# Performance work log

Measured on AMD Instinct MI355X. Metric: run time of the kernel, lower is better.

The kernel has to match this reference:

```python
import jax, jax.numpy as jnp
import numpy as np

B, N = 262144, 64
CLIP_RATIO = 0.2
DUAL_CLIP = 5.0
USE_VALUE_CLIP = True
HALF_LOG_2PI = 0.5 * float(np.log(2.0 * np.pi))


def setup_inputs() -> dict:
    key = jax.random.key(0)
    ks = jax.random.split(key, 9)
    return {
        "mu_new": jax.random.normal(ks[0], (B, N), jnp.float32),
        "sigma_new": jax.random.uniform(ks[1], (B, N), jnp.float32, 0.5, 1.5),
        "mu_old": jax.random.normal(ks[2], (B, N), jnp.float32),
        "sigma_old": jax.random.uniform(ks[3], (B, N), jnp.float32, 0.5, 1.5),
        "action": jax.random.normal(ks[4], (B, N), jnp.float32),
        "value_new": jax.random.normal(ks[5], (B,), jnp.float32),
        "value_old": jax.random.normal(ks[6], (B,), jnp.float32),
        "adv": jax.random.normal(ks[7], (B,), jnp.float32),
        "return_": jax.random.normal(ks[8], (B,), jnp.float32),
        "weight": jnp.ones((B,), jnp.float32),
    }


def _gauss_logprob(action, mu, sigma):
    # independent Normal log-prob, summed over action dim -> (B,)
    z = (action - mu) / sigma
    return jnp.sum(-0.5 * z * z - jnp.log(sigma) - HALF_LOG_2PI, axis=-1)


def reference(mu_new, sigma_new, mu_old, sigma_old, action,
              value_new, value_old, adv, return_, weight):
    logp_new = _gauss_logprob(action, mu_new, sigma_new)   # (B,)
    logp_old = _gauss_logprob(action, mu_old, sigma_old)   # (B,) constant w.r.t. new params
    ratio = jnp.exp(logp_new - logp_old)

    surr1 = ratio * adv
    surr2 = jnp.clip(ratio, 1.0 - CLIP_RATIO, 1.0 + CLIP_RATIO) * adv
    clipped = jnp.minimum(surr1, surr2)
    # dual clip (arXiv:1912.09729 Eq. 5)
    clipped = jnp.maximum(clipped, DUAL_CLIP * adv)
    policy_loss = -jnp.mean(clipped * weight)

    # entropy of diagonal Gaussian, summed over N
    entropy = jnp.sum(0.5 + HALF_LOG_2PI + jnp.log(sigma_new), axis=-1)
    entropy_loss = jnp.mean(entropy * weight)

    if USE_VALUE_CLIP:
        value_clip = value_old + jnp.clip(value_new - value_old, -CLIP_RATIO, CLIP_RATIO)
        v1 = jnp.square(return_ - value_new)
        v2 = jnp.square(return_ - value_clip)
        value_loss = 0.5 * jnp.mean(jnp.maximum(v1, v2) * weight)
    else:
        value_loss = 0.5 * jnp.mean(jnp.square(return_ - value_new) * weight)

    approx_kl = jnp.mean(logp_old - logp_new)
    clipfrac = jnp.mean((jnp.abs(ratio - 1.0) > CLIP_RATIO).astype(jnp.float32))
    return policy_loss, value_loss, entropy_loss, approx_kl, clipfrac
```

## Files before the change

### kernel.cpp

```cpp
#include <hip/hip_runtime.h>

static constexpr int   N_DIM        = 64;
static constexpr float HALF_LOG_2PI = 0.9189385332046727f;
static constexpr float CLIP_RATIO   = 0.2f;
static constexpr float DUAL_CLIP    = 5.0f;
static constexpr int   GRID         = 2048;

__global__ __launch_bounds__(256) void ppo_main(
    const float* __restrict__ mu_new,
    const float* __restrict__ sg_new,
    const float* __restrict__ mu_old,
    const float* __restrict__ sg_old,
    const float* __restrict__ act,
    const float* __restrict__ vnew,
    const float* __restrict__ vold,
    const float* __restrict__ adv,
    const float* __restrict__ ret,
    const float* __restrict__ wgt,
    float* __restrict__ ws,
    int n_groups, int b_rows)
{
    const int t    = threadIdx.x;
    const int wave = t >> 6;
    const int lane = t & 63;
    const int sub  = lane >> 4;
    const int sl   = lane & 15;

    float accP = 0.f, accV = 0.f, accE = 0.f, accK = 0.f, accC = 0.f;

    {
        const int gtid = blockIdx.x * 256 + t;
        const int tot  = gridDim.x * 256;
        for (int r = gtid; r < b_rows; r += tot) {
            const float vn = vnew[r], vo = vold[r], rt = ret[r], w = wgt[r];
            const float vc = vo + fminf(fmaxf(vn - vo, -CLIP_RATIO), CLIP_RATIO);
            const float d1 = rt - vn, d2 = rt - vc;
            accV += fmaxf(d1 * d1, d2 * d2) * w;
        }
    }

    for (int g = blockIdx.x; g < n_groups; g += gridDim.x) {
        const int base_row = g * 16 + wave * 4;
        const int off      = base_row * N_DIM + lane * 4;

        const float4 mn = *(const float4*)(mu_new + off);
        const float4 sn = *(const float4*)(sg_new + off);
        const float4 mo = *(const float4*)(mu_old + off);
        const float4 so = *(const float4*)(sg_old + off);
        const float4 a  = *(const float4*)(act    + off);

        float w = 0.f, ad = 0.f;
        if (sl == 0) {
            const int r = base_row + sub;
            w  = wgt[r];
            ad = adv[r];
        }

        float qn = 0.f, qo = 0.f, en = 0.f, eo = 0.f;
#define PPO_COMP(c) {                                        \
        float rn = __builtin_amdgcn_rcpf(sn.c);              \
        float zn = (a.c - mn.c) * rn;  qn += zn * zn;        \
        float ro = __builtin_amdgcn_rcpf(so.c);              \
        float zo = (a.c - mo.c) * ro;  qo += zo * zo;        \
        en += __logf(sn.c);  eo += __logf(so.c); }
        PPO_COMP(x) PPO_COMP(y) PPO_COMP(z) PPO_COMP(w)
#undef PPO_COMP

        float pn = -0.5f * qn - en;
        float po = -0.5f * qo - eo;

#pragma unroll
        for (int m = 1; m < 16; m <<= 1) {
            pn += __shfl_xor(pn, m, 16);
            po += __shfl_xor(po, m, 16);
            en += __shfl_xor(en, m, 16);
        }

        if (sl == 0) {
            const float ratio = __expf(pn - po);
            const float s1 = ratio * ad;
            const float rc = fminf(fmaxf(ratio, 1.0f - CLIP_RATIO), 1.0f + CLIP_RATIO);
            const float s2 = rc * ad;
            float cl = fminf(s1, s2);
            cl = fmaxf(cl, DUAL_CLIP * ad);
            accP += cl * w;

            accE += ((float)N_DIM * (0.5f + HALF_LOG_2PI) + en) * w;
            accK += (po - pn);
            accC += (fabsf(ratio - 1.0f) > CLIP_RATIO) ? 1.0f : 0.0f;
        }
    }

#pragma unroll
    for (int m = 1; m < 64; m <<= 1) accV += __shfl_xor(accV, m, 64);
#pragma unroll
    for (int m = 16; m < 64; m <<= 1) {
        accP += __shfl_xor(accP, m, 64);
        accE += __shfl_xor(accE, m, 64);
        accK += __shfl_xor(accK, m, 64);
        accC += __shfl_xor(accC, m, 64);
    }

    __shared__ float red[4][5];
    if (lane == 0) {
        red[wave][0] = accP; red[wave][1] = accV; red[wave][2] = accE;
        red[wave][3] = accK; red[wave][4] = accC;
    }
    __syncthreads();

    if (t == 0) {
        float s[5] = {0.f, 0.f, 0.f, 0.f, 0.f};
#pragma unroll
        for (int wv = 0; wv < 4; ++wv)
#pragma unroll
            for (int k = 0; k < 5; ++k) s[k] += red[wv][k];
#pragma unroll
        for (int k = 0; k < 5; ++k) ws[k * GRID + blockIdx.x] = s[k];
    }
}

__global__ __launch_bounds__(256) void ppo_reduce(
    const float* __restrict__ ws, float* __restrict__ out, int b_rows)
{
    const int t    = threadIdx.x;
    const int wave = t >> 6;
    const int lane = t & 63;
    __shared__ float red[4];

    const float invB = 1.0f / (float)b_rows;

    for (int k = 0; k < 5; ++k) {
        float v = 0.f;
        for (int i = t; i < GRID; i += 256) v += ws[k * GRID + i];
#pragma unroll
        for (int m = 1; m < 64; m <<= 1) v += __shfl_xor(v, m, 64);
        if (lane == 0) red[wave] = v;
        __syncthreads();
        if (t == 0) {
            float s = red[0] + red[1] + red[2] + red[3];
            float o;
            if      (k == 0) o = -s * invB;
            else if (k == 1) o = 0.5f * s * invB;
            else             o = s * invB;
            out[k] = o;
        }
        __syncthreads();
    }
}

extern "C" void kernel_launch(void* const* d_in, const int* in_sizes, int n_in,
                              void* d_out, int out_size, void* d_ws, size_t ws_size,
                              hipStream_t stream) {
    const float* mu_new = (const float*)d_in[0];
    const float* sg_new = (const float*)d_in[1];
    const float* mu_old = (const float*)d_in[2];
    const float* sg_old = (const float*)d_in[3];
    const float* act    = (const float*)d_in[4];
    const float* vnew   = (const float*)d_in[5];
    const float* vold   = (const float*)d_in[6];
    const float* adv    = (const float*)d_in[7];
    const float* ret    = (const float*)d_in[8];
    const float* wgt    = (const float*)d_in[9];
    float* out = (float*)d_out;
    float* ws  = (float*)d_ws;

    const int b_rows   = in_sizes[5];
    const int n_groups = b_rows / 16;

    ppo_main<<<GRID, 256, 0, stream>>>(mu_new, sg_new, mu_old, sg_old, act,
                                       vnew, vold, adv, ret, wgt,
                                       ws, n_groups, b_rows);
    ppo_reduce<<<1, 256, 0, stream>>>(ws, out, b_rows);
}
```

Measured before the change: 322.9 us.

## Process two row sets per iteration and cut shuffle reductions in PPO loss

Each wave now handles 8 rows per loop iteration instead of 4, issuing ten float4 loads at once to put more memory requests in flight. Only the log-ratio difference goes through the 16-lane shuffle reduction. Entropy and KL are accumulated per lane, and the ratio terms are computed redundantly on all lanes, then scaled by 1/16. The value-loss loop becomes a single guarded pass, which assumes the grid covers every row. The final reduce kernel uses one wave per output instead of looping with barriers.

```diff
diff --git a/kernel.cpp b/kernel.cpp
--- a/kernel.cpp
+++ b/kernel.cpp
@@ -5,6 +5,26 @@
 static constexpr float CLIP_RATIO   = 0.2f;
 static constexpr float DUAL_CLIP    = 5.0f;
 static constexpr int   GRID         = 2048;
+static constexpr float ENT_CONST    = (float)N_DIM * (0.5f + HALF_LOG_2PI);
+static constexpr float ENT_C16      = ENT_CONST / 16.0f;
+
+__device__ __forceinline__ void ppo_set(const float4& mn, const float4& sn,
+                                        const float4& mo, const float4& so,
+                                        const float4& a,
+                                        float& en_out, float& d_out)
+{
+    float qn = 0.f, qo = 0.f, en = 0.f, eo = 0.f;
+#define PPO_COMP(c) {                                        \
+        float rn = __builtin_amdgcn_rcpf(sn.c);              \
+        float zn = (a.c - mn.c) * rn;  qn += zn * zn;        \
+        float ro = __builtin_amdgcn_rcpf(so.c);              \
+        float zo = (a.c - mo.c) * ro;  qo += zo * zo;        \
+        en += __logf(sn.c);  eo += __logf(so.c); }
+    PPO_COMP(x) PPO_COMP(y) PPO_COMP(z) PPO_COMP(w)
+#undef PPO_COMP
+    en_out = en;
+    d_out  = 0.5f * (qo - qn) + (eo - en);
+}
 
 __global__ __launch_bounds__(256) void ppo_main(
     const float* __restrict__ mu_new,
@@ -18,20 +38,18 @@
     const float* __restrict__ ret,
     const float* __restrict__ wgt,
     float* __restrict__ ws,
-    int n_groups, int b_rows)
+    int b_rows)
 {
     const int t    = threadIdx.x;
     const int wave = t >> 6;
     const int lane = t & 63;
     const int sub  = lane >> 4;
-    const int sl   = lane & 15;
 
     float accP = 0.f, accV = 0.f, accE = 0.f, accK = 0.f, accC = 0.f;
 
     {
-        const int gtid = blockIdx.x * 256 + t;
-        const int tot  = gridDim.x * 256;
-        for (int r = gtid; r < b_rows; r += tot) {
+        const int r = blockIdx.x * 256 + t;
+        if (r < b_rows) {
             const float vn = vnew[r], vo = vold[r], rt = ret[r], w = wgt[r];
             const float vc = vo + fminf(fmaxf(vn - vo, -CLIP_RATIO), CLIP_RATIO);
             const float d1 = rt - vn, d2 = rt - vc;
@@ -39,63 +57,65 @@
         }
     }
 
-    for (int g = blockIdx.x; g < n_groups; g += gridDim.x) {
-        const int base_row = g * 16 + wave * 4;
-        const int off      = base_row * N_DIM + lane * 4;
+    const int n_g = b_rows >> 5;
+    for (int g = blockIdx.x; g < n_g; g += gridDim.x) {
+        const int row0 = g * 32 + wave * 8;
+        const int r0   = row0 + sub;
+        const int r1   = r0 + 4;
+        const int off0 = row0 * N_DIM + lane * 4;
+        const int off1 = off0 + 4 * N_DIM;
 
-        const float4 mn = *(const float4*)(mu_new + off);
-        const float4 sn = *(const float4*)(sg_new + off);
-        const float4 mo = *(const float4*)(mu_old + off);
-        const float4 so = *(const float4*)(sg_old + off);
-        const float4 a  = *(const float4*)(act    + off);
+        const float4 mn0 = *(const float4*)(mu_new + off0);
+        const float4 sn0 = *(const float4*)(sg_new + off0);
+        const float4 mo0 = *(const float4*)(mu_old + off0);
+        const float4 so0 = *(const float4*)(sg_old + off0);
+        const float4 a0  = *(const float4*)(act    + off0);
+        const float4 mn1 = *(const float4*)(mu_new + off1);
+        const float4 sn1 = *(const float4*)(sg_new + off1);
+        const float4 mo1 = *(const float4*)(mu_old + off1);
+        const float4 so1 = *(const float4*)(sg_old + off1);
+        const float4 a1  = *(const float4*)(act    + off1);
+        const float w0 = wgt[r0], ad0 = adv[r0];
+        const float w1 = wgt[r1], ad1 = adv[r1];
 
-        float w = 0.f, ad = 0.f;
-        if (sl == 0) {
-            const int r = base_row + sub;
-            w  = wgt[r];
-            ad = adv[r];
-        }
+        float en0, d0, en1, d1;
+        ppo_set(mn0, sn0, mo0, so0, a0, en0, d0);
+        ppo_set(mn1, sn1, mo1, so1, a1, en1, d1);
 
-        float qn = 0.f, qo = 0.f, en = 0.f, eo = 0.f;
-#define PPO_COMP(c) {                                        \
-        float rn = __builtin_amdgcn_rcpf(sn.c);              \
-        float zn = (a.c - mn.c) * rn;  qn += zn * zn;        \
-        float ro = __builtin_amdgcn_rcpf(so.c);              \
-        float zo = (a.c - mo.c) * ro;  qo += zo * zo;        \
-        en += __logf(sn.c);  eo += __logf(so.c); }
-        PPO_COMP(x) PPO_COMP(y) PPO_COMP(z) PPO_COMP(w)
-#undef PPO_COMP
-
-        float pn = -0.5f * qn - en;
-        float po = -0.5f * qo - eo;
+        accK -= (d0 + d1);
+        accE += w0 * (en0 + ENT_C16) + w1 * (en1 + ENT_C16);
 
 #pragma unroll
         for (int m = 1; m < 16; m <<= 1) {
-            pn += __shfl_xor(pn, m, 16);
-            po += __shfl_xor(po, m, 16);
-            en += __shfl_xor(en, m, 16);
+            d0 += __shfl_xor(d0, m, 16);
+            d1 += __shfl_xor(d1, m, 16);
         }
 
-        if (sl == 0) {
-            const float ratio = __expf(pn - po);
-            const float s1 = ratio * ad;
-            const float rc = fminf(fmaxf(ratio, 1.0f - CLIP_RATIO), 1.0f + CLIP_RATIO);
-            const float s2 = rc * ad;
-            float cl = fminf(s1, s2);
-            cl = fmaxf(cl, DUAL_CLIP * ad);
-            accP += cl * w;
-
-            accE += ((float)N_DIM * (0.5f + HALF_LOG_2PI) + en) * w;
-            accK += (po - pn);
-            accC += (fabsf(ratio - 1.0f) > CLIP_RATIO) ? 1.0f : 0.0f;
+        {
+            const float ratio = __expf(d0);
+            const float rc = fminf(fmaxf(ratio, 1.f - CLIP_RATIO), 1.f + CLIP_RATIO);
+            float cl = fminf(ratio * ad0, rc * ad0);
+            cl = fmaxf(cl, DUAL_CLIP * ad0);
+            accP += cl * w0;
+            accC += (fabsf(ratio - 1.f) > CLIP_RATIO) ? 1.f : 0.f;
+        }
+        {
+            const float ratio = __expf(d1);
+            const float rc = fminf(fmaxf(ratio, 1.f - CLIP_RATIO), 1.f + CLIP_RATIO);
+            float cl = fminf(ratio * ad1, rc * ad1);
+            cl = fmaxf(cl, DUAL_CLIP * ad1);
+            accP += cl * w1;
+            accC += (fabsf(ratio - 1.f) > CLIP_RATIO) ? 1.f : 0.f;
         }
     }
 
+    accP *= 0.0625f;
+    accC *= 0.0625f;
+
 #pragma unroll
-    for (int m = 1; m < 64; m <<= 1) accV += __shfl_xor(accV, m, 64);
-#pragma unroll
-    for (int m = 16; m < 64; m <<= 1) {
+    for (int m = 1; m < 64; m <<= 1) {
         accP += __shfl_xor(accP, m, 64);
+        accV += __shfl_xor(accV, m, 64);
         accE += __shfl_xor(accE, m, 64);
         accK += __shfl_xor(accK, m, 64);
         accC += __shfl_xor(accC, m, 64);
@@ -119,32 +139,24 @@
     }
 }
 
-__global__ __launch_bounds__(256) void ppo_reduce(
+__global__ __launch_bounds__(320) void ppo_reduce(
     const float* __restrict__ ws, float* __restrict__ out, int b_rows)
 {
-    const int t    = threadIdx.x;
-    const int wave = t >> 6;
-    const int lane = t & 63;
-    __shared__ float red[4];
+    const int wave = threadIdx.x >> 6;
+    const int lane = threadIdx.x & 63;
 
-    const float invB = 1.0f / (float)b_rows;
+    float v = 0.f;
+    for (int i = lane; i < GRID; i += 64) v += ws[wave * GRID + i];
+#pragma unroll
+    for (int m = 1; m < 64; m <<= 1) v += __shfl_xor(v, m, 64);
 
-    for (int k = 0; k < 5; ++k) {
-        float v = 0.f;
-        for (int i = t; i < GRID; i += 256) v += ws[k * GRID + i];
-#pragma unroll
-        for (int m = 1; m < 64; m <<= 1) v += __shfl_xor(v, m, 64);
-        if (lane == 0) red[wave] = v;
-        __syncthreads();
-        if (t == 0) {
-            float s = red[0] + red[1] + red[2] + red[3];
-            float o;
-            if      (k == 0) o = -s * invB;
-            else if (k == 1) o = 0.5f * s * invB;
-            else             o = s * invB;
-            out[k] = o;
-        }
-        __syncthreads();
+    if (lane == 0) {
+        const float invB = 1.0f / (float)b_rows;
+        float o;
+        if      (wave == 0) o = -v * invB;
+        else if (wave == 1) o = 0.5f * v * invB;
+        else                o = v * invB;
+        out[wave] = o;
     }
 }
 
@@ -164,11 +176,10 @@
     float* out = (float*)d_out;
     float* ws  = (float*)d_ws;
 
-    const int b_rows   = in_sizes[5];
-    const int n_groups = b_rows / 16;
+    const int b_rows = in_sizes[5];
 
     ppo_main<<<GRID, 256, 0, stream>>>(mu_new, sg_new, mu_old, sg_old, act,
                                        vnew, vold, adv, ret, wgt,
-                                       ws, n_groups, b_rows);
-    ppo_reduce<<<1, 256, 0, stream>>>(ws, out, b_rows);
+                                       ws, b_rows);
+    ppo_reduce<<<1, 320, 0, stream>>>(ws, out, b_rows);
 }
```

After: 315.5 us. 2.3% less time.
